# Performance work log

Hardware: AMD Instinct MI355X
Metric: run time of the kernel (lower is better)

The kernel has to match this reference:

```python
import jax, jax.numpy as jnp
import numpy as np

B, T, E = 4, 2048, 1024
H, HS = 16, 64
FF = 4 * E
EPS = 1e-5


def _layer_norm(x, g, b):
    mu = jnp.mean(x, axis=-1, keepdims=True)
    var = jnp.mean(jnp.square(x - mu), axis=-1, keepdims=True)
    return (x - mu) * jax.lax.rsqrt(var + EPS) * g + b


def setup_inputs() -> dict:
    key = jax.random.key(0)
    ks = jax.random.split(key, 8)
    s_e = 1.0 / np.sqrt(E)
    s_hs = 1.0 / np.sqrt(H * HS)
    s_ff = 1.0 / np.sqrt(FF)
    return {
        "x": jax.random.normal(ks[0], (B, T, E), dtype=jnp.float32),
        # weights stored as [in, out] (transpose of torch's [out, in])
        "qkv_w": jax.random.uniform(ks[1], (E, 3 * H * HS), minval=-s_e, maxval=s_e),
        "attn_proj_w": jax.random.uniform(ks[2], (H * HS, E), minval=-s_hs, maxval=s_hs),
        "attn_proj_b": jax.random.uniform(ks[3], (E,), minval=-s_hs, maxval=s_hs),
        "ln1_g": jnp.ones((E,), jnp.float32),
        "ln1_b": jnp.zeros((E,), jnp.float32),
        "ln2_g": jnp.ones((E,), jnp.float32),
        "ln2_b": jnp.zeros((E,), jnp.float32),
        "ff_w1": jax.random.uniform(ks[4], (E, FF), minval=-s_e, maxval=s_e),
        "ff_b1": jax.random.uniform(ks[5], (FF,), minval=-s_e, maxval=s_e),
        "ff_w2": jax.random.uniform(ks[6], (FF, E), minval=-s_ff, maxval=s_ff),
        "ff_b2": jax.random.uniform(ks[7], (E,), minval=-s_ff, maxval=s_ff),
    }


def reference(x, qkv_w, attn_proj_w, attn_proj_b, ln1_g, ln1_b, ln2_g, ln2_b,
              ff_w1, ff_b1, ff_w2, ff_b2):
    b, t, _ = x.shape
    # --- pre-LN causal self-attention ---
    h = _layer_norm(x, ln1_g, ln1_b)
    qkv = h @ qkv_w                                  # [B,T,3*H*HS]
    q, k, v = jnp.split(qkv, 3, axis=-1)
    q = q.reshape(b, t, H, HS).transpose(0, 2, 1, 3)  # [B,H,T,HS]
    k = k.reshape(b, t, H, HS).transpose(0, 2, 1, 3)
    v = v.reshape(b, t, H, HS).transpose(0, 2, 1, 3)
    scores = jnp.einsum('bhqd,bhkd->bhqk', q, k) * (HS ** -0.5)
    causal = jnp.tril(jnp.ones((t, t), dtype=bool))
    scores = jnp.where(causal, scores, -jnp.inf)
    attn = jax.nn.softmax(scores, axis=-1)
    out = jnp.einsum('bhqk,bhkd->bhqd', attn, v)      # [B,H,T,HS]
    out = out.transpose(0, 2, 1, 3).reshape(b, t, H * HS)
    x = x + out @ attn_proj_w + attn_proj_b
    # --- pre-LN feed-forward ---
    h2 = _layer_norm(x, ln2_g, ln2_b)
    ff = jax.nn.relu(h2 @ ff_w1 + ff_b1) @ ff_w2 + ff_b2
    return x + ff
```

## Files before the change

### kernel.cpp

```cpp
#include <hip/hip_runtime.h>
#include <math.h>

#define B_ 4
#define T_ 2048
#define E_ 1024
#define H_ 16
#define HS_ 64
#define FF_ 4096
#define M_ (B_ * T_)
#define QKV3_ (3 * H_ * HS_)

typedef short bf16x8 __attribute__((ext_vector_type(8)));
typedef float f32x4 __attribute__((ext_vector_type(4)));

__device__ __forceinline__ unsigned short f2bf(float f) {
    unsigned int u = __float_as_uint(f);
    return (unsigned short)((u + 0x7fffu + ((u >> 16) & 1u)) >> 16);
}
__device__ __forceinline__ float bf2f(unsigned short h) {
    return __uint_as_float(((unsigned int)h) << 16);
}

__device__ __forceinline__ void gload16(const void* g, void* l) {
    __builtin_amdgcn_global_load_lds(
        (const __attribute__((address_space(1))) void*)g,
        (__attribute__((address_space(3))) void*)l, 16, 0, 0);
}

__global__ __launch_bounds__(256) void wT_bf16(const float* __restrict__ W,
                                               unsigned short* __restrict__ WT,
                                               int K, int N) {
    __shared__ float t[32][33];
    const int n0 = blockIdx.x * 32, k0 = blockIdx.y * 32;
    const int tid = threadIdx.x;
#pragma unroll
    for (int i = 0; i < 4; i++) {
        const int idx = i * 256 + tid;
        const int r = idx >> 5, c = idx & 31;
        t[r][c] = W[(size_t)(k0 + r) * N + n0 + c];
    }
    __syncthreads();
#pragma unroll
    for (int i = 0; i < 4; i++) {
        const int idx = i * 256 + tid;
        const int n = idx >> 5, k = idx & 31;
        WT[(size_t)(n0 + n) * K + k0 + k] = f2bf(t[k][n]);
    }
}

__global__ __launch_bounds__(256) void ln_bf16(const float* __restrict__ x,
                                               const float* __restrict__ g,
                                               const float* __restrict__ b,
                                               unsigned short* __restrict__ out) {
    const int row = blockIdx.x;
    const int tid = threadIdx.x;
    const float4 v = ((const float4*)(x + (size_t)row * E_))[tid];
    float s = v.x + v.y + v.z + v.w;
    float ss = v.x * v.x + v.y * v.y + v.z * v.z + v.w * v.w;
    for (int off = 32; off > 0; off >>= 1) {
        s += __shfl_down(s, off);
        ss += __shfl_down(ss, off);
    }
    __shared__ float rs[4], rss[4];
    const int wid = tid >> 6;
    if ((tid & 63) == 0) { rs[wid] = s; rss[wid] = ss; }
    __syncthreads();
    const float tot = rs[0] + rs[1] + rs[2] + rs[3];
    const float tot2 = rss[0] + rss[1] + rss[2] + rss[3];
    const float mean = tot * (1.0f / E_);
    const float var = tot2 * (1.0f / E_) - mean * mean;
    const float rstd = rsqrtf(var + 1e-5f);
    const float4 gv = ((const float4*)g)[tid];
    const float4 bv = ((const float4*)b)[tid];
    ushort4 o;
    o.x = f2bf((v.x - mean) * rstd * gv.x + bv.x);
    o.y = f2bf((v.y - mean) * rstd * gv.y + bv.y);
    o.z = f2bf((v.z - mean) * rstd * gv.z + bv.z);
    o.w = f2bf((v.w - mean) * rstd * gv.w + bv.w);
    ((ushort4*)(out + (size_t)row * E_))[tid] = o;
}

template <bool BIASF, bool RELU, bool RES, bool OUTBF16>
__global__ __launch_bounds__(256) void gemm_bf16(
    const unsigned short* __restrict__ A,
    const unsigned short* __restrict__ BT,
    const float* __restrict__ bias,
    const float* __restrict__ res,
    float* __restrict__ Cf,
    unsigned short* __restrict__ Cb,
    int M, int N, int K) {
    __shared__ unsigned short Al[128 * 32];
    __shared__ unsigned short Bl[128 * 32];

    const int tid = threadIdx.x;
    const int lane = tid & 63;
    const int w = tid >> 6;
    const int wm = w >> 1, wn = w & 1;
    const int rowBase = blockIdx.y * 128, colBase = blockIdx.x * 128;

    f32x4 acc[4][4];
#pragma unroll
    for (int mt = 0; mt < 4; mt++)
#pragma unroll
        for (int nt = 0; nt < 4; nt++)
#pragma unroll
            for (int r = 0; r < 4; r++) acc[mt][nt][r] = 0.0f;

    const size_t rA = (size_t)rowBase * K;
    const size_t rB = (size_t)colBase * K;
    const int lm = lane & 15;
    const int kgo = (lane >> 4) * 16;

    for (int k0 = 0; k0 < K; k0 += 32) {
#pragma unroll
        for (int i = 0; i < 2; i++) {
            const int c = (w * 2 + i) * 64 + lane;
            const int r = c >> 2, kc = c & 3;
            gload16(A + rA + (size_t)r * K + k0 + kc * 8, (char*)Al + c * 16);
            gload16(BT + rB + (size_t)r * K + k0 + kc * 8, (char*)Bl + c * 16);
        }
        __syncthreads();

        bf16x8 af[4], bfr[4];
#pragma unroll
        for (int mt = 0; mt < 4; mt++)
            af[mt] = *(const bf16x8*)((const char*)Al + (wm * 64 + mt * 16 + lm) * 64 + kgo);
#pragma unroll
        for (int nt = 0; nt < 4; nt++)
            bfr[nt] = *(const bf16x8*)((const char*)Bl + (wn * 64 + nt * 16 + lm) * 64 + kgo);
#pragma unroll
        for (int mt = 0; mt < 4; mt++)
#pragma unroll
            for (int nt = 0; nt < 4; nt++)
                acc[mt][nt] = __builtin_amdgcn_mfma_f32_16x16x32_bf16(
                    af[mt], bfr[nt], acc[mt][nt], 0, 0, 0);
        __syncthreads();
    }

#pragma unroll
    for (int mt = 0; mt < 4; mt++) {
#pragma unroll
        for (int nt = 0; nt < 4; nt++) {
            const int cg = colBase + wn * 64 + nt * 16 + lm;
#pragma unroll
            for (int r = 0; r < 4; r++) {
                const int rg = rowBase + wm * 64 + mt * 16 + (lane >> 4) * 4 + r;
                float v = acc[mt][nt][r];
                if (BIASF) v += bias[cg];
                if (RELU) v = fmaxf(v, 0.0f);
                if (RES) v += res[(size_t)rg * N + cg];
                if (OUTBF16) Cb[(size_t)rg * N + cg] = f2bf(v);
                else Cf[(size_t)rg * N + cg] = v;
            }
        }
    }
}

__global__ __launch_bounds__(256) void attn_mfma(const unsigned short* __restrict__ qkv,
                                                 unsigned short* __restrict__ out) {
    __shared__ unsigned short Ks[32 * 72];
    __shared__ unsigned short Vs[32 * 72];

    const int tid = threadIdx.x;
    const int lane = tid & 63;
    const int w = tid >> 6;
    const int qt = blockIdx.x;
    const int bh = blockIdx.y;
    const int b = bh >> 4, h = bh & 15;
    const int bT = b * T_;
    const int q0w = qt * 64 + w * 16;
    const int lm = lane & 15;
    const int kg = lane >> 4;

    const size_t qoff = (size_t)(bT + q0w + lm) * QKV3_ + h * HS_;
    const bf16x8 qf0 = *(const bf16x8*)(qkv + qoff + kg * 8);
    const bf16x8 qf1 = *(const bf16x8*)(qkv + qoff + 32 + kg * 8);

    f32x4 o[4];
#pragma unroll
    for (int dt = 0; dt < 4; dt++)
#pragma unroll
        for (int r = 0; r < 4; r++) o[dt][r] = 0.0f;
    float mrun = -INFINITY, lrun = 0.0f;

    const int ntiles = 2 * qt + 2;
    for (int kt = 0; kt < ntiles; kt++) {
        const int kvbase = kt * 32;
        __syncthreads();
        {
            const int r = tid >> 3, ch = tid & 7;
            const size_t krow = (size_t)(bT + kvbase + r) * QKV3_ + h * HS_ + ch * 8;
            *(bf16x8*)(Ks + r * 72 + ch * 8) = *(const bf16x8*)(qkv + krow + E_);
            *(bf16x8*)(Vs + r * 72 + ch * 8) = *(const bf16x8*)(qkv + krow + 2 * E_);
        }
        __syncthreads();
        if (kvbase > q0w + 15) continue;

        f32x4 z;
        z[0] = z[1] = z[2] = z[3] = 0.0f;
        const bf16x8 a00 = *(const bf16x8*)(Ks + (lm)*72 + kg * 8);
        const bf16x8 a01 = *(const bf16x8*)(Ks + (lm)*72 + 32 + kg * 8);
        const bf16x8 a10 = *(const bf16x8*)(Ks + (16 + lm) * 72 + kg * 8);
        const bf16x8 a11 = *(const bf16x8*)(Ks + (16 + lm) * 72 + 32 + kg * 8);
        f32x4 s0 = __builtin_amdgcn_mfma_f32_16x16x32_bf16(a00, qf0, z, 0, 0, 0);
        s0 = __builtin_amdgcn_mfma_f32_16x16x32_bf16(a01, qf1, s0, 0, 0, 0);
        f32x4 s1 = __builtin_amdgcn_mfma_f32_16x16x32_bf16(a10, qf0, z, 0, 0, 0);
        s1 = __builtin_amdgcn_mfma_f32_16x16x32_bf16(a11, qf1, s1, 0, 0, 0);

        const int qg = q0w + lm;
        float sv[8];
#pragma unroll
        for (int r = 0; r < 4; r++) {
            const int kv0 = kvbase + kg * 4 + r;
            sv[r] = (kv0 <= qg) ? s0[r] * 0.125f : -INFINITY;
            sv[4 + r] = (kv0 + 16 <= qg) ? s1[r] * 0.125f : -INFINITY;
        }
        float mx = sv[0];
#pragma unroll
        for (int j = 1; j < 8; j++) mx = fmaxf(mx, sv[j]);
        mx = fmaxf(mx, __shfl_xor(mx, 16));
        mx = fmaxf(mx, __shfl_xor(mx, 32));
        const float mnew = fmaxf(mrun, mx);
        const float alpha = __expf(mrun - mnew);
        float p[8], ls = 0.0f;
#pragma unroll
        for (int j = 0; j < 8; j++) {
            p[j] = __expf(sv[j] - mnew);
            ls += p[j];
        }
        ls += __shfl_xor(ls, 16);
        ls += __shfl_xor(ls, 32);
        lrun = lrun * alpha + ls;
        mrun = mnew;

        bf16x8 pa;
#pragma unroll
        for (int j = 0; j < 8; j++) ((unsigned short*)&pa)[j] = f2bf(p[j]);

#pragma unroll
        for (int r = 0; r < 4; r++) {
            const float ar = __shfl(alpha, kg * 4 + r);
#pragma unroll
            for (int dt = 0; dt < 4; dt++) o[dt][r] *= ar;
        }

#pragma unroll
        for (int dt = 0; dt < 4; dt++) {
            bf16x8 vf;
#pragma unroll
            for (int j = 0; j < 8; j++) {
                const int kvl = kg * 4 + (j & 3) + 16 * (j >> 2);
                ((unsigned short*)&vf)[j] = Vs[kvl * 72 + dt * 16 + lm];
            }
            o[dt] = __builtin_amdgcn_mfma_f32_16x16x32_bf16(pa, vf, o[dt], 0, 0, 0);
        }
    }

#pragma unroll
    for (int r = 0; r < 4; r++) {
        const float li = 1.0f / __shfl(lrun, kg * 4 + r);
        const size_t rowo = (size_t)(bT + q0w + kg * 4 + r) * E_ + h * HS_;
#pragma unroll
        for (int dt = 0; dt < 4; dt++)
            out[rowo + dt * 16 + lm] = f2bf(o[dt][r] * li);
    }
}

extern "C" void kernel_launch(void* const* d_in, const int* in_sizes, int n_in,
                              void* d_out, int out_size, void* d_ws, size_t ws_size,
                              hipStream_t stream) {
    const float* x           = (const float*)d_in[0];
    const float* qkv_w       = (const float*)d_in[1];
    const float* attn_proj_w = (const float*)d_in[2];
    const float* attn_proj_b = (const float*)d_in[3];
    const float* ln1_g       = (const float*)d_in[4];
    const float* ln1_b       = (const float*)d_in[5];
    const float* ln2_g       = (const float*)d_in[6];
    const float* ln2_b       = (const float*)d_in[7];
    const float* ff_w1       = (const float*)d_in[8];
    const float* ff_b1       = (const float*)d_in[9];
    const float* ff_w2       = (const float*)d_in[10];
    const float* ff_b2       = (const float*)d_in[11];
    float* out = (float*)d_out;
    char* wsb = (char*)d_ws;

    unsigned short* wqkvT  = (unsigned short*)(wsb + 0);
    unsigned short* wprojT = (unsigned short*)(wsb + 6291456);
    unsigned short* wff1T  = (unsigned short*)(wsb + 8388608);
    unsigned short* wff2T  = (unsigned short*)(wsb + 16777216);
    unsigned short* hbuf   = (unsigned short*)(wsb + 25165824);
    unsigned short* attnb  = (unsigned short*)(wsb + 41943040);
    unsigned short* qkvb   = (unsigned short*)(wsb + 58720256);
    unsigned short* ff1b   = qkvb;

    wT_bf16<<<dim3(QKV3_ / 32, E_ / 32), 256, 0, stream>>>(qkv_w, wqkvT, E_, QKV3_);
    wT_bf16<<<dim3(E_ / 32, E_ / 32), 256, 0, stream>>>(attn_proj_w, wprojT, E_, E_);
    wT_bf16<<<dim3(FF_ / 32, E_ / 32), 256, 0, stream>>>(ff_w1, wff1T, E_, FF_);
    wT_bf16<<<dim3(E_ / 32, FF_ / 32), 256, 0, stream>>>(ff_w2, wff2T, FF_, E_);

    ln_bf16<<<M_, 256, 0, stream>>>(x, ln1_g, ln1_b, hbuf);
    gemm_bf16<false, false, false, true><<<dim3(QKV3_ / 128, M_ / 128), 256, 0, stream>>>(
        hbuf, wqkvT, nullptr, nullptr, nullptr, qkvb, M_, QKV3_, E_);
    attn_mfma<<<dim3(T_ / 64, B_ * H_), 256, 0, stream>>>(qkvb, attnb);
    gemm_bf16<true, false, true, false><<<dim3(E_ / 128, M_ / 128), 256, 0, stream>>>(
        attnb, wprojT, attn_proj_b, x, out, nullptr, M_, E_, E_);
    ln_bf16<<<M_, 256, 0, stream>>>(out, ln2_g, ln2_b, hbuf);
    gemm_bf16<true, true, false, true><<<dim3(FF_ / 128, M_ / 128), 256, 0, stream>>>(
        hbuf, wff1T, ff_b1, nullptr, nullptr, ff1b, M_, FF_, E_);
    gemm_bf16<true, false, true, false><<<dim3(E_ / 128, M_ / 128), 256, 0, stream>>>(
        ff1b, wff2T, ff_b2, out, out, nullptr, M_, E_, FF_);
    (void)ws_size; (void)in_sizes; (void)n_in; (void)out_size;
}
```

Measured before the change: 672.5 us.

## Deepen GEMM K-tile with swizzled LDS and rewrite attention with larger tiles

The GEMM now stages a K=64 slice per iteration into XOR-swizzled LDS and remaps workgroup IDs across 8 groups for better cache locality. Attention is rewritten so each block covers 128 queries, with 32 per wave and 64-key tiles. It prefetches K/V into registers, stores V transposed in LDS and runs the softmax in exp2 form with a skipped rescale when the running max barely changes. The heaviest causal blocks are launched first. This is meant to cut synchronisation and LDS bank conflicts and raise MFMA density, at the cost of more LDS and registers and a lazy-rescale bound that limits how large unnormalised values can grow.

```diff
diff --git a/kernel.cpp b/kernel.cpp
--- a/kernel.cpp
+++ b/kernel.cpp
@@ -11,14 +11,12 @@
 #define QKV3_ (3 * H_ * HS_)
 
 typedef short bf16x8 __attribute__((ext_vector_type(8)));
+typedef short bf16x4 __attribute__((ext_vector_type(4)));
 typedef float f32x4 __attribute__((ext_vector_type(4)));
 
 __device__ __forceinline__ unsigned short f2bf(float f) {
     unsigned int u = __float_as_uint(f);
     return (unsigned short)((u + 0x7fffu + ((u >> 16) & 1u)) >> 16);
-}
-__device__ __forceinline__ float bf2f(unsigned short h) {
-    return __uint_as_float(((unsigned int)h) << 16);
 }
 
 __device__ __forceinline__ void gload16(const void* g, void* l) {
@@ -89,14 +87,20 @@
     float* __restrict__ Cf,
     unsigned short* __restrict__ Cb,
     int M, int N, int K) {
-    __shared__ unsigned short Al[128 * 32];
-    __shared__ unsigned short Bl[128 * 32];
+    __shared__ unsigned short Al[128 * 64];
+    __shared__ unsigned short Bl[128 * 64];
 
     const int tid = threadIdx.x;
     const int lane = tid & 63;
     const int w = tid >> 6;
     const int wm = w >> 1, wn = w & 1;
-    const int rowBase = blockIdx.y * 128, colBase = blockIdx.x * 128;
+
+    const int gx = gridDim.x;
+    const int nwg = gx * gridDim.y;
+    const int lin = blockIdx.y * gx + blockIdx.x;
+    const int cpx = nwg >> 3;
+    const int swz = (lin & 7) * cpx + (lin >> 3);
+    const int rowBase = (swz / gx) * 128, colBase = (swz % gx) * 128;
 
     f32x4 acc[4][4];
 #pragma unroll
@@ -109,31 +113,37 @@
     const size_t rA = (size_t)rowBase * K;
     const size_t rB = (size_t)colBase * K;
     const int lm = lane & 15;
-    const int kgo = (lane >> 4) * 16;
-
-    for (int k0 = 0; k0 < K; k0 += 32) {
-#pragma unroll
-        for (int i = 0; i < 2; i++) {
-            const int c = (w * 2 + i) * 64 + lane;
-            const int r = c >> 2, kc = c & 3;
-            gload16(A + rA + (size_t)r * K + k0 + kc * 8, (char*)Al + c * 16);
-            gload16(BT + rB + (size_t)r * K + k0 + kc * 8, (char*)Bl + c * 16);
+    const int kg = lane >> 4;
+
+    for (int k0 = 0; k0 < K; k0 += 64) {
+#pragma unroll
+        for (int i = 0; i < 4; i++) {
+            const int c = (w * 4 + i) * 64 + lane;
+            const int r = c >> 3, s = c & 7;
+            const int ss = s ^ (r & 7);
+            gload16(A + rA + (size_t)r * K + k0 + ss * 8, (char*)Al + c * 16);
+            gload16(BT + rB + (size_t)r * K + k0 + ss * 8, (char*)Bl + c * 16);
         }
         __syncthreads();
 
-        bf16x8 af[4], bfr[4];
-#pragma unroll
-        for (int mt = 0; mt < 4; mt++)
-            af[mt] = *(const bf16x8*)((const char*)Al + (wm * 64 + mt * 16 + lm) * 64 + kgo);
-#pragma unroll
-        for (int nt = 0; nt < 4; nt++)
-            bfr[nt] = *(const bf16x8*)((const char*)Bl + (wn * 64 + nt * 16 + lm) * 64 + kgo);
-#pragma unroll
-        for (int mt = 0; mt < 4; mt++)
+#pragma unroll
+        for (int ks = 0; ks < 2; ks++) {
+            bf16x8 af[4], bfr[4];
+#pragma unroll
+            for (int mt = 0; mt < 4; mt++)
+                af[mt] = *(const bf16x8*)(Al + (wm * 64 + mt * 16 + lm) * 64 +
+                                          (((ks * 4 + kg) ^ (lm & 7)) * 8));
 #pragma unroll
             for (int nt = 0; nt < 4; nt++)
-                acc[mt][nt] = __builtin_amdgcn_mfma_f32_16x16x32_bf16(
-                    af[mt], bfr[nt], acc[mt][nt], 0, 0, 0);
+                bfr[nt] = *(const bf16x8*)(Bl + (wn * 64 + nt * 16 + lm) * 64 +
+                                           (((ks * 4 + kg) ^ (lm & 7)) * 8));
+#pragma unroll
+            for (int mt = 0; mt < 4; mt++)
+#pragma unroll
+                for (int nt = 0; nt < 4; nt++)
+                    acc[mt][nt] = __builtin_amdgcn_mfma_f32_16x16x32_bf16(
+                        af[mt], bfr[nt], acc[mt][nt], 0, 0, 0);
+        }
         __syncthreads();
     }
 
@@ -144,7 +154,7 @@
             const int cg = colBase + wn * 64 + nt * 16 + lm;
 #pragma unroll
             for (int r = 0; r < 4; r++) {
-                const int rg = rowBase + wm * 64 + mt * 16 + (lane >> 4) * 4 + r;
+                const int rg = rowBase + wm * 64 + mt * 16 + kg * 4 + r;
                 float v = acc[mt][nt][r];
                 if (BIASF) v += bias[cg];
                 if (RELU) v = fmaxf(v, 0.0f);
@@ -156,114 +166,170 @@
     }
 }
 
-__global__ __launch_bounds__(256) void attn_mfma(const unsigned short* __restrict__ qkv,
-                                                 unsigned short* __restrict__ out) {
-    __shared__ unsigned short Ks[32 * 72];
-    __shared__ unsigned short Vs[32 * 72];
+__global__ __launch_bounds__(256) void attn_mfma2(const unsigned short* __restrict__ qkv,
+                                                  unsigned short* __restrict__ out) {
+    __shared__ unsigned short Ks[64 * 64];
+    __shared__ unsigned short Vt[64 * 72];
 
     const int tid = threadIdx.x;
     const int lane = tid & 63;
     const int w = tid >> 6;
-    const int qt = blockIdx.x;
+    const int lm = lane & 15;
+    const int kg = lane >> 4;
+    const int qt = 15 - blockIdx.x;
     const int bh = blockIdx.y;
     const int b = bh >> 4, h = bh & 15;
     const int bT = b * T_;
-    const int q0w = qt * 64 + w * 16;
-    const int lm = lane & 15;
-    const int kg = lane >> 4;
-
-    const size_t qoff = (size_t)(bT + q0w + lm) * QKV3_ + h * HS_;
-    const bf16x8 qf0 = *(const bf16x8*)(qkv + qoff + kg * 8);
-    const bf16x8 qf1 = *(const bf16x8*)(qkv + qoff + 32 + kg * 8);
-
-    f32x4 o[4];
-#pragma unroll
-    for (int dt = 0; dt < 4; dt++)
-#pragma unroll
-        for (int r = 0; r < 4; r++) o[dt][r] = 0.0f;
-    float mrun = -INFINITY, lrun = 0.0f;
-
-    const int ntiles = 2 * qt + 2;
-    for (int kt = 0; kt < ntiles; kt++) {
-        const int kvbase = kt * 32;
+    const int q0w = qt * 128 + w * 32;
+    const float K1 = 0.18033688011f;
+
+    bf16x8 qf[2][2];
+#pragma unroll
+    for (int qg = 0; qg < 2; qg++) {
+        const size_t qo = (size_t)(bT + q0w + qg * 16 + lm) * QKV3_ + h * HS_;
+#pragma unroll
+        for (int dc = 0; dc < 2; dc++)
+            qf[qg][dc] = *(const bf16x8*)(qkv + qo + dc * 32 + kg * 8);
+    }
+
+    f32x4 o[2][4];
+#pragma unroll
+    for (int qg = 0; qg < 2; qg++)
+#pragma unroll
+        for (int dt = 0; dt < 4; dt++)
+#pragma unroll
+            for (int r = 0; r < 4; r++) o[qg][dt][r] = 0.0f;
+    float m2[2] = {-INFINITY, -INFINITY};
+    float l[2] = {0.0f, 0.0f};
+
+    const int rK = tid >> 3, chK = tid & 7;
+    const int sK = (chK ^ (rK & 7)) * 8;
+    const int rp = tid >> 3, chV = tid & 7;
+    const int vws = (2 * rp) ^ (chV << 2);
+
+    const size_t hK = E_ + h * HS_;
+    const size_t hV = 2 * E_ + h * HS_;
+    bf16x8 kA, kB, vA, vB;
+
+#define LOADT(kvb)                                                                          \
+    do {                                                                                    \
+        kA = *(const bf16x8*)(qkv + (size_t)(bT + (kvb) + rK) * QKV3_ + hK + chK * 8);      \
+        kB = *(const bf16x8*)(qkv + (size_t)(bT + (kvb) + rK + 32) * QKV3_ + hK + chK * 8); \
+        vA = *(const bf16x8*)(qkv + (size_t)(bT + (kvb) + 2 * rp) * QKV3_ + hV + chV * 8);  \
+        vB = *(const bf16x8*)(qkv + (size_t)(bT + (kvb) + 2 * rp + 1) * QKV3_ + hV + chV * 8); \
+    } while (0)
+
+    const int nt = 2 * (qt + 1);
+    LOADT(0);
+    for (int t = 0; t < nt; t++) {
+        const int kvbase = t * 64;
         __syncthreads();
-        {
-            const int r = tid >> 3, ch = tid & 7;
-            const size_t krow = (size_t)(bT + kvbase + r) * QKV3_ + h * HS_ + ch * 8;
-            *(bf16x8*)(Ks + r * 72 + ch * 8) = *(const bf16x8*)(qkv + krow + E_);
-            *(bf16x8*)(Vs + r * 72 + ch * 8) = *(const bf16x8*)(qkv + krow + 2 * E_);
-        }
+        *(bf16x8*)(Ks + rK * 64 + sK) = kA;
+        *(bf16x8*)(Ks + (rK + 32) * 64 + sK) = kB;
+#pragma unroll
+        for (int i = 0; i < 8; i++) {
+            const unsigned int pv = (unsigned int)(unsigned short)vA[i] |
+                                    ((unsigned int)(unsigned short)vB[i] << 16);
+            *(unsigned int*)(Vt + (chV * 8 + i) * 72 + vws) = pv;
+        }
+        if (t + 1 < nt) LOADT((t + 1) * 64);
         __syncthreads();
-        if (kvbase > q0w + 15) continue;
-
-        f32x4 z;
-        z[0] = z[1] = z[2] = z[3] = 0.0f;
-        const bf16x8 a00 = *(const bf16x8*)(Ks + (lm)*72 + kg * 8);
-        const bf16x8 a01 = *(const bf16x8*)(Ks + (lm)*72 + 32 + kg * 8);
-        const bf16x8 a10 = *(const bf16x8*)(Ks + (16 + lm) * 72 + kg * 8);
-        const bf16x8 a11 = *(const bf16x8*)(Ks + (16 + lm) * 72 + 32 + kg * 8);
-        f32x4 s0 = __builtin_amdgcn_mfma_f32_16x16x32_bf16(a00, qf0, z, 0, 0, 0);
-        s0 = __builtin_amdgcn_mfma_f32_16x16x32_bf16(a01, qf1, s0, 0, 0, 0);
-        f32x4 s1 = __builtin_amdgcn_mfma_f32_16x16x32_bf16(a10, qf0, z, 0, 0, 0);
-        s1 = __builtin_amdgcn_mfma_f32_16x16x32_bf16(a11, qf1, s1, 0, 0, 0);
-
-        const int qg = q0w + lm;
-        float sv[8];
+        if (kvbase > q0w + 31) continue;
+
+        bf16x8 af[4][2];
+#pragma unroll
+        for (int g = 0; g < 4; g++)
+#pragma unroll
+            for (int dc = 0; dc < 2; dc++)
+                af[g][dc] = *(const bf16x8*)(Ks + (g * 16 + lm) * 64 +
+                                             (((dc * 4 + kg) ^ (lm & 7)) * 8));
+
+        bf16x8 pa[2][2];
+#pragma unroll
+        for (int qg = 0; qg < 2; qg++) {
+            f32x4 z = {0.0f, 0.0f, 0.0f, 0.0f};
+            f32x4 s[4];
+#pragma unroll
+            for (int g = 0; g < 4; g++) {
+                s[g] = __builtin_amdgcn_mfma_f32_16x16x32_bf16(af[g][0], qf[qg][0], z, 0, 0, 0);
+                s[g] = __builtin_amdgcn_mfma_f32_16x16x32_bf16(af[g][1], qf[qg][1], s[g], 0, 0, 0);
+            }
+            const int qrow = q0w + qg * 16 + lm;
+            float sv[16];
+#pragma unroll
+            for (int g = 0; g < 4; g++)
+#pragma unroll
+                for (int r = 0; r < 4; r++) sv[g * 4 + r] = s[g][r];
+            if (kvbase + 63 > q0w + qg * 16) {
+#pragma unroll
+                for (int g = 0; g < 4; g++)
+#pragma unroll
+                    for (int r = 0; r < 4; r++) {
+                        const int kv = kvbase + g * 16 + kg * 4 + r;
+                        if (kv > qrow) sv[g * 4 + r] = -INFINITY;
+                    }
+            }
+            float mx = sv[0];
+#pragma unroll
+            for (int j = 1; j < 16; j++) mx = fmaxf(mx, sv[j]);
+            mx = fmaxf(mx, __shfl_xor(mx, 16));
+            mx = fmaxf(mx, __shfl_xor(mx, 32));
+            const float mx2 = mx * K1;
+            if (!__all(m2[qg] > -1e30f && mx2 <= m2[qg] + 11.5f)) {
+                const float m2new = fmaxf(m2[qg], mx2);
+                const float alpha = exp2f(m2[qg] - m2new);
+#pragma unroll
+                for (int r = 0; r < 4; r++) {
+                    const float ar = __shfl(alpha, kg * 4 + r);
+#pragma unroll
+                    for (int dt = 0; dt < 4; dt++) o[qg][dt][r] *= ar;
+                }
+                l[qg] *= alpha;
+                m2[qg] = m2new;
+            }
+            float p[16], ls = 0.0f;
+#pragma unroll
+            for (int j = 0; j < 16; j++) {
+                p[j] = exp2f(fmaf(sv[j], K1, -m2[qg]));
+                ls += p[j];
+            }
+            ls += __shfl_xor(ls, 16);
+            ls += __shfl_xor(ls, 32);
+            l[qg] += ls;
+#pragma unroll
+            for (int j = 0; j < 8; j++) {
+                ((unsigned short*)&pa[qg][0])[j] = f2bf(p[j]);
+                ((unsigned short*)&pa[qg][1])[j] = f2bf(p[8 + j]);
+            }
+        }
+
+#pragma unroll
+        for (int dt = 0; dt < 4; dt++) {
+            const int drow = dt * 16 + lm;
+            const unsigned short* vrow = Vt + drow * 72;
+            const int xo = (kg * 4) ^ (((drow >> 3) & 7) << 2);
+#pragma unroll
+            for (int c = 0; c < 2; c++) {
+                const bf16x4 lo = *(const bf16x4*)(vrow + c * 32 + xo);
+                const bf16x4 hi = *(const bf16x4*)(vrow + c * 32 + (xo ^ 16));
+                const bf16x8 vf = __builtin_shufflevector(lo, hi, 0, 1, 2, 3, 4, 5, 6, 7);
+                o[0][dt] = __builtin_amdgcn_mfma_f32_16x16x32_bf16(pa[0][c], vf, o[0][dt], 0, 0, 0);
+                o[1][dt] = __builtin_amdgcn_mfma_f32_16x16x32_bf16(pa[1][c], vf, o[1][dt], 0, 0, 0);
+            }
+        }
+    }
+#undef LOADT
+
+#pragma unroll
+    for (int qg = 0; qg < 2; qg++)
 #pragma unroll
         for (int r = 0; r < 4; r++) {
-            const int kv0 = kvbase + kg * 4 + r;
-            sv[r] = (kv0 <= qg) ? s0[r] * 0.125f : -INFINITY;
-            sv[4 + r] = (kv0 + 16 <= qg) ? s1[r] * 0.125f : -INFINITY;
-        }
-        float mx = sv[0];
-#pragma unroll
-        for (int j = 1; j < 8; j++) mx = fmaxf(mx, sv[j]);
-        mx = fmaxf(mx, __shfl_xor(mx, 16));
-        mx = fmaxf(mx, __shfl_xor(mx, 32));
-        const float mnew = fmaxf(mrun, mx);
-        const float alpha = __expf(mrun - mnew);
-        float p[8], ls = 0.0f;
-#pragma unroll
-        for (int j = 0; j < 8; j++) {
-            p[j] = __expf(sv[j] - mnew);
-            ls += p[j];
-        }
-        ls += __shfl_xor(ls, 16);
-        ls += __shfl_xor(ls, 32);
-        lrun = lrun * alpha + ls;
-        mrun = mnew;
-
-        bf16x8 pa;
-#pragma unroll
-        for (int j = 0; j < 8; j++) ((unsigned short*)&pa)[j] = f2bf(p[j]);
-
-#pragma unroll
-        for (int r = 0; r < 4; r++) {
-            const float ar = __shfl(alpha, kg * 4 + r);
-#pragma unroll
-            for (int dt = 0; dt < 4; dt++) o[dt][r] *= ar;
-        }
-
-#pragma unroll
-        for (int dt = 0; dt < 4; dt++) {
-            bf16x8 vf;
-#pragma unroll
-            for (int j = 0; j < 8; j++) {
-                const int kvl = kg * 4 + (j & 3) + 16 * (j >> 2);
-                ((unsigned short*)&vf)[j] = Vs[kvl * 72 + dt * 16 + lm];
-            }
-            o[dt] = __builtin_amdgcn_mfma_f32_16x16x32_bf16(pa, vf, o[dt], 0, 0, 0);
-        }
-    }
-
-#pragma unroll
-    for (int r = 0; r < 4; r++) {
-        const float li = 1.0f / __shfl(lrun, kg * 4 + r);
-        const size_t rowo = (size_t)(bT + q0w + kg * 4 + r) * E_ + h * HS_;
-#pragma unroll
-        for (int dt = 0; dt < 4; dt++)
-            out[rowo + dt * 16 + lm] = f2bf(o[dt][r] * li);
-    }
+            const float li = 1.0f / __shfl(l[qg], kg * 4 + r);
+            const size_t ro = (size_t)(bT + q0w + qg * 16 + kg * 4 + r) * E_ + h * HS_;
+#pragma unroll
+            for (int dt = 0; dt < 4; dt++)
+                out[ro + dt * 16 + lm] = f2bf(o[qg][dt][r] * li);
+        }
 }
 
 extern "C" void kernel_launch(void* const* d_in, const int* in_sizes, int n_in,
@@ -301,7 +367,7 @@
     ln_bf16<<<M_, 256, 0, stream>>>(x, ln1_g, ln1_b, hbuf);
     gemm_bf16<false, false, false, true><<<dim3(QKV3_ / 128, M_ / 128), 256, 0, stream>>>(
         hbuf, wqkvT, nullptr, nullptr, nullptr, qkvb, M_, QKV3_, E_);
-    attn_mfma<<<dim3(T_ / 64, B_ * H_), 256, 0, stream>>>(qkvb, attnb);
+    attn_mfma2<<<dim3(T_ / 128, B_ * H_), 256, 0, stream>>>(qkvb, attnb);
     gemm_bf16<true, false, true, false><<<dim3(E_ / 128, M_ / 128), 256, 0, stream>>>(
         attnb, wprojT, attn_proj_b, x, out, nullptr, M_, E_, E_);
     ln_bf16<<<M_, 256, 0, stream>>>(out, ln2_g, ln2_b, hbuf);
```

Result: faster. 586.8 us (-12.7%).
